# Kernel tuning notes

Measured on AMD Instinct MI355X. Metric: run time of the kernel, lower is better.

The kernel has to match this reference:

```python
import jax, jax.numpy as jnp
import numpy as np

N, E, G = 50000, 800000, 100
H, C = 4, 64


def _gatv2(x, src, dst, ea, Wl, bl, Wr, br, We, att, bias):
    # PyG GATv2Conv: x_l = lin_l(x) (source side), x_r = lin_r(x) (target side)
    xl = (x @ Wl + bl).reshape(-1, H, C)
    xr = (x @ Wr + br).reshape(-1, H, C)
    e = (ea @ We).reshape(-1, H, C)               # [E,H,C]
    m = jax.nn.leaky_relu(xl[src] + xr[dst] + e, negative_slope=0.2)
    alpha = jnp.einsum('ehc,hc->eh', m, att)      # [E,H]
    amax = jax.ops.segment_max(alpha, dst, num_segments=N)
    amax = jnp.where(jnp.isfinite(amax), amax, jnp.float32(0.0))
    ex = jnp.exp(alpha - amax[dst])
    denom = jax.ops.segment_sum(ex, dst, num_segments=N)
    a = ex / (denom[dst] + jnp.float32(1e-16))    # segment softmax over in-edges
    out = jax.ops.segment_sum(xl[src] * a[..., None], dst, num_segments=N)
    return out.reshape(N, H * C) + bias


def setup_inputs() -> dict:
    key = jax.random.key(0)
    ks = jax.random.split(key, 24)
    lin = lambda k, i, o: (jax.random.normal(k, (i, o), jnp.float32) / np.sqrt(i).astype(np.float32))
    x = jax.random.normal(ks[0], (N, 8), jnp.float32)
    edge_index = jnp.stack([jax.random.randint(ks[1], (E,), 0, N),
                            jax.random.randint(ks[2], (E,), 0, N)])
    edge_attr = jax.random.normal(ks[3], (E, 1), jnp.float32)
    batch = jnp.sort(jax.random.randint(ks[4], (N,), 0, G))
    return dict(
        x=x, edge_index=edge_index, edge_attr=edge_attr, batch=batch,
        enc_W=lin(ks[5], 8, 64), enc_b=jnp.zeros((64,), jnp.float32),
        g1_Wl=lin(ks[6], 64, 256), g1_bl=jnp.zeros((256,), jnp.float32),
        g1_Wr=lin(ks[7], 64, 256), g1_br=jnp.zeros((256,), jnp.float32),
        g1_We=lin(ks[8], 1, 256),
        g1_att=jax.random.normal(ks[9], (H, C), jnp.float32) / np.sqrt(C).astype(np.float32),
        g1_bias=jnp.zeros((256,), jnp.float32),
        g2_Wl=lin(ks[10], 256, 256), g2_bl=jnp.zeros((256,), jnp.float32),
        g2_Wr=lin(ks[11], 256, 256), g2_br=jnp.zeros((256,), jnp.float32),
        g2_We=lin(ks[12], 1, 256),
        g2_att=jax.random.normal(ks[13], (H, C), jnp.float32) / np.sqrt(C).astype(np.float32),
        g2_bias=jnp.zeros((256,), jnp.float32),
        p1_W=lin(ks[14], 256, 128), p1_b=jnp.zeros((128,), jnp.float32),
        ln_g=jnp.ones((128,), jnp.float32), ln_b=jnp.zeros((128,), jnp.float32),
        p2_W=lin(ks[15], 128, 64), p2_b=jnp.zeros((64,), jnp.float32),
    )


def reference(x, edge_index, edge_attr, batch,
              enc_W, enc_b,
              g1_Wl, g1_bl, g1_Wr, g1_br, g1_We, g1_att, g1_bias,
              g2_Wl, g2_bl, g2_Wr, g2_br, g2_We, g2_att, g2_bias,
              p1_W, p1_b, ln_g, ln_b, p2_W, p2_b):
    src, dst = edge_index[0], edge_index[1]
    h = jax.nn.relu(x @ enc_W + enc_b)
    h = jax.nn.relu(_gatv2(h, src, dst, edge_attr, g1_Wl, g1_bl, g1_Wr, g1_br, g1_We, g1_att, g1_bias))
    h = jax.nn.relu(_gatv2(h, src, dst, edge_attr, g2_Wl, g2_bl, g2_Wr, g2_br, g2_We, g2_att, g2_bias))
    # global mean pool over graphs
    sums = jax.ops.segment_sum(h, batch, num_segments=G)
    cnt = jax.ops.segment_sum(jnp.ones((N, 1), h.dtype), batch, num_segments=G)
    p = sums / jnp.maximum(cnt, jnp.float32(1.0))
    # post MLP (dropout is identity in eval)
    z = p @ p1_W + p1_b
    mu = jnp.mean(z, axis=-1, keepdims=True)
    var = jnp.mean(jnp.square(z - mu), axis=-1, keepdims=True)
    z = (z - mu) * jax.lax.rsqrt(var + jnp.float32(1e-5)) * ln_g + ln_b
    z = jax.nn.relu(z)
    return jax.nn.relu(z @ p2_W + p2_b)
```

## Files before the change

kernel.cpp:

```cpp
#include <hip/hip_runtime.h>
#include <hip/hip_fp16.h>

#define NH 4
#define CH 64

__global__ void encoder_kernel(const float* __restrict__ x, const float* __restrict__ W,
                               const float* __restrict__ b, float* __restrict__ h, int N) {
  int idx = blockIdx.x * blockDim.x + threadIdx.x;
  if (idx >= N * 64) return;
  int n = idx >> 6, j = idx & 63;
  const float* xp = x + n * 8;
  float acc = b[j];
#pragma unroll
  for (int k = 0; k < 8; ++k) acc = fmaf(xp[k], W[k * 64 + j], acc);
  h[idx] = fmaxf(acc, 0.0f);
}

template <int K>
__global__ void lin_lr_kernel(const float* __restrict__ h,
                              const float* __restrict__ Wl, const float* __restrict__ bl,
                              const float* __restrict__ Wr, const float* __restrict__ br,
                              __half* __restrict__ xl, float* __restrict__ xr, int N) {
  __shared__ float hs[8][K];
  int n0 = blockIdx.x * 8;
  int j = threadIdx.x;
  int nmax = N - n0; if (nmax > 8) nmax = 8;
  for (int idx = j; idx < nmax * K; idx += 256) {
    int m = idx / K, k = idx % K;
    hs[m][k] = h[(size_t)(n0 + m) * K + k];
  }
  __syncthreads();
  float accl[8], accr[8];
  float bjl = bl[j], bjr = br[j];
#pragma unroll
  for (int m = 0; m < 8; ++m) { accl[m] = bjl; accr[m] = bjr; }
  for (int k = 0; k < K; ++k) {
    float wl = Wl[k * 256 + j];
    float wr = Wr[k * 256 + j];
#pragma unroll
    for (int m = 0; m < 8; ++m) {
      accl[m] = fmaf(hs[m][k], wl, accl[m]);
      accr[m] = fmaf(hs[m][k], wr, accr[m]);
    }
  }
  for (int m = 0; m < nmax; ++m) {
    xl[(size_t)(n0 + m) * 256 + j] = __float2half_rn(accl[m]);
    xr[(size_t)(n0 + m) * 256 + j] = accr[m];
  }
}

__global__ void hist_kernel(const int* __restrict__ dst, int* __restrict__ deg, int E) {
  int e = blockIdx.x * blockDim.x + threadIdx.x;
  if (e < E) atomicAdd(&deg[dst[e]], 1);
}

__global__ void scan_partial_kernel(const int* __restrict__ deg, int* __restrict__ partial, int N) {
  __shared__ int sm[256];
  int t = threadIdx.x;
  int i = blockIdx.x * 256 + t;
  sm[t] = (i < N) ? deg[i] : 0;
  __syncthreads();
#pragma unroll
  for (int s = 128; s > 0; s >>= 1) {
    if (t < s) sm[t] += sm[t + s];
    __syncthreads();
  }
  if (t == 0) partial[blockIdx.x] = sm[0];
}

__global__ void scan_offsets_kernel(int* __restrict__ partial, int nb) {
  __shared__ int sm[256];
  int t = threadIdx.x;
  int v = (t < nb) ? partial[t] : 0;
  sm[t] = v;
  __syncthreads();
#pragma unroll
  for (int off = 1; off < 256; off <<= 1) {
    int a = (t >= off) ? sm[t - off] : 0;
    __syncthreads();
    sm[t] += a;
    __syncthreads();
  }
  if (t < nb) partial[t] = sm[t] - v;
}

__global__ void scan_final_kernel(const int* __restrict__ deg, const int* __restrict__ partial,
                                  int* __restrict__ rowptr, int* __restrict__ cursor, int N, int E) {
  __shared__ int sm[256];
  int t = threadIdx.x;
  int i = blockIdx.x * 256 + t;
  int v = (i < N) ? deg[i] : 0;
  sm[t] = v;
  __syncthreads();
#pragma unroll
  for (int off = 1; off < 256; off <<= 1) {
    int a = (t >= off) ? sm[t - off] : 0;
    __syncthreads();
    sm[t] += a;
    __syncthreads();
  }
  if (i < N) {
    int ex = partial[blockIdx.x] + sm[t] - v;
    rowptr[i] = ex;
    cursor[i] = ex;
  }
  if (i == 0) rowptr[N] = E;
}

__global__ void scatter_build_kernel(const int* __restrict__ src, const int* __restrict__ dst,
                                     const float* __restrict__ ea, int* __restrict__ cursor,
                                     int* __restrict__ srcs, float* __restrict__ eas, int E) {
  int e = blockIdx.x * blockDim.x + threadIdx.x;
  if (e >= E) return;
  int d = dst[e];
  int pos = atomicAdd(&cursor[d], 1);
  srcs[pos] = src[e];
  eas[pos] = ea[e];
}

__device__ __forceinline__ float4 ldxl(const uint2* __restrict__ xlh, int s, int lane) {
  uint2 r = xlh[(size_t)s * 64 + lane];
  __half2 a = *reinterpret_cast<const __half2*>(&r.x);
  __half2 b = *reinterpret_cast<const __half2*>(&r.y);
  float2 fa = __half22float2(a);
  float2 fb = __half22float2(b);
  return make_float4(fa.x, fa.y, fb.x, fb.y);
}

__device__ __forceinline__ void edge_accum(const float4 xlv, const float eav,
                                           const float4 xr4, const float4 We4, const float4 at4,
                                           float4& acc, float& denom) {
  float4 v;
  v.x = fmaf(eav, We4.x, xlv.x + xr4.x);
  v.y = fmaf(eav, We4.y, xlv.y + xr4.y);
  v.z = fmaf(eav, We4.z, xlv.z + xr4.z);
  v.w = fmaf(eav, We4.w, xlv.w + xr4.w);
  v.x = (v.x >= 0.f) ? v.x : 0.2f * v.x;
  v.y = (v.y >= 0.f) ? v.y : 0.2f * v.y;
  v.z = (v.z >= 0.f) ? v.z : 0.2f * v.z;
  v.w = (v.w >= 0.f) ? v.w : 0.2f * v.w;
  float p = v.x * at4.x + v.y * at4.y + v.z * at4.z + v.w * at4.w;
  p += __shfl_xor(p, 1, 64);
  p += __shfl_xor(p, 2, 64);
  p += __shfl_xor(p, 4, 64);
  p += __shfl_xor(p, 8, 64);
  float ex = __expf(p);
  denom += ex;
  acc.x = fmaf(ex, xlv.x, acc.x);
  acc.y = fmaf(ex, xlv.y, acc.y);
  acc.z = fmaf(ex, xlv.z, acc.z);
  acc.w = fmaf(ex, xlv.w, acc.w);
}

template <bool POOL>
__global__ void gat_aggregate_kernel(const int* __restrict__ rowptr,
                                     const int* __restrict__ srcs,
                                     const float* __restrict__ eas,
                                     const __half* __restrict__ xl,
                                     const float* __restrict__ xr,
                                     const float* __restrict__ We,
                                     const float* __restrict__ att,
                                     const float* __restrict__ bias,
                                     float* __restrict__ out,
                                     const int* __restrict__ batch,
                                     float* __restrict__ sums,
                                     float* __restrict__ cnt,
                                     int N) {
  int d = (int)((blockIdx.x * (size_t)blockDim.x + threadIdx.x) >> 6);
  int lane = threadIdx.x & 63;
  if (d >= N) return;
  const uint2* xlh = (const uint2*)xl;
  float4 xr4 = ((const float4*)xr)[(size_t)d * 64 + lane];
  float4 We4 = ((const float4*)We)[lane];
  float4 at4 = ((const float4*)att)[lane];
  int beg = rowptr[d], end = rowptr[d + 1];
  float4 acc = {0.f, 0.f, 0.f, 0.f};
  float denom = 0.f;
  int i = beg;
  for (; i + 7 < end; i += 8) {
    int s[8]; float ev[8];
#pragma unroll
    for (int k = 0; k < 8; ++k) { s[k] = srcs[i + k]; ev[k] = eas[i + k]; }
    float4 a[8];
#pragma unroll
    for (int k = 0; k < 8; ++k) a[k] = ldxl(xlh, s[k], lane);
#pragma unroll
    for (int k = 0; k < 8; ++k) edge_accum(a[k], ev[k], xr4, We4, at4, acc, denom);
  }
  for (; i + 3 < end; i += 4) {
    int s[4]; float ev[4];
#pragma unroll
    for (int k = 0; k < 4; ++k) { s[k] = srcs[i + k]; ev[k] = eas[i + k]; }
    float4 a[4];
#pragma unroll
    for (int k = 0; k < 4; ++k) a[k] = ldxl(xlh, s[k], lane);
#pragma unroll
    for (int k = 0; k < 4; ++k) edge_accum(a[k], ev[k], xr4, We4, at4, acc, denom);
  }
  for (; i < end; ++i) {
    float4 a0 = ldxl(xlh, srcs[i], lane);
    edge_accum(a0, eas[i], xr4, We4, at4, acc, denom);
  }
  float inv = 1.f / (denom + 1e-16f);
  float4 b4 = ((const float4*)bias)[lane];
  float4 o;
  o.x = fmaxf(fmaf(acc.x, inv, b4.x), 0.f);
  o.y = fmaxf(fmaf(acc.y, inv, b4.y), 0.f);
  o.z = fmaxf(fmaf(acc.z, inv, b4.z), 0.f);
  o.w = fmaxf(fmaf(acc.w, inv, b4.w), 0.f);
  if (POOL) {
    int g = batch[d];
    float* sg = sums + (size_t)g * 256 + lane * 4;
    atomicAdd(sg + 0, o.x);
    atomicAdd(sg + 1, o.y);
    atomicAdd(sg + 2, o.z);
    atomicAdd(sg + 3, o.w);
    if (lane == 0) atomicAdd(&cnt[g], 1.0f);
  } else {
    ((float4*)out)[(size_t)d * 64 + lane] = o;
  }
}

__global__ void mlp_kernel(const float* __restrict__ sums, const float* __restrict__ cnt,
                           const float* __restrict__ p1W, const float* __restrict__ p1b,
                           const float* __restrict__ lng, const float* __restrict__ lnb,
                           const float* __restrict__ p2W, const float* __restrict__ p2b,
                           float* __restrict__ outp, int G) {
  __shared__ float p[256];
  __shared__ float z[128];
  __shared__ float wsum[2];
  __shared__ float wsum2[2];
  int g = blockIdx.x;
  int t = threadIdx.x;
  float c = fmaxf(cnt[g], 1.0f);
  p[t] = sums[(size_t)g * 256 + t] / c;
  p[t + 128] = sums[(size_t)g * 256 + t + 128] / c;
  __syncthreads();
  float acc = p1b[t];
  for (int k = 0; k < 256; ++k) acc = fmaf(p[k], p1W[k * 128 + t], acc);
  float v = acc;
#pragma unroll
  for (int off = 32; off > 0; off >>= 1) v += __shfl_xor(v, off, 64);
  if ((t & 63) == 0) wsum[t >> 6] = v;
  __syncthreads();
  float mu = (wsum[0] + wsum[1]) * (1.0f / 128.0f);
  float dv = acc - mu;
  float vv = dv * dv;
#pragma unroll
  for (int off = 32; off > 0; off >>= 1) vv += __shfl_xor(vv, off, 64);
  if ((t & 63) == 0) wsum2[t >> 6] = vv;
  __syncthreads();
  float var = (wsum2[0] + wsum2[1]) * (1.0f / 128.0f);
  float zv = dv * rsqrtf(var + 1e-5f) * lng[t] + lnb[t];
  z[t] = fmaxf(zv, 0.0f);
  __syncthreads();
  if (t < 64) {
    float o = p2b[t];
    for (int k = 0; k < 128; ++k) o = fmaf(z[k], p2W[k * 64 + t], o);
    outp[(size_t)g * 64 + t] = fmaxf(o, 0.0f);
  }
}

extern "C" void kernel_launch(void* const* d_in, const int* in_sizes, int n_in,
                              void* d_out, int out_size, void* d_ws, size_t ws_size,
                              hipStream_t stream) {
  const float* x      = (const float*)d_in[0];
  const int*   ei     = (const int*)d_in[1];
  const float* ea     = (const float*)d_in[2];
  const int*   batch  = (const int*)d_in[3];
  const float* enc_W  = (const float*)d_in[4];
  const float* enc_b  = (const float*)d_in[5];
  const float* Wl1    = (const float*)d_in[6];
  const float* bl1    = (const float*)d_in[7];
  const float* Wr1    = (const float*)d_in[8];
  const float* br1    = (const float*)d_in[9];
  const float* We1    = (const float*)d_in[10];
  const float* att1   = (const float*)d_in[11];
  const float* bias1  = (const float*)d_in[12];
  const float* Wl2    = (const float*)d_in[13];
  const float* bl2    = (const float*)d_in[14];
  const float* Wr2    = (const float*)d_in[15];
  const float* br2    = (const float*)d_in[16];
  const float* We2    = (const float*)d_in[17];
  const float* att2   = (const float*)d_in[18];
  const float* bias2  = (const float*)d_in[19];
  const float* p1W    = (const float*)d_in[20];
  const float* p1b    = (const float*)d_in[21];
  const float* lng    = (const float*)d_in[22];
  const float* lnb    = (const float*)d_in[23];
  const float* p2W    = (const float*)d_in[24];
  const float* p2b    = (const float*)d_in[25];
  float* outp = (float*)d_out;

  int N = in_sizes[0] / 8;
  int E = in_sizes[2];
  int G = out_size / 64;
  const int* src = ei;
  const int* dst = ei + E;
  int nb = (N + 255) / 256;

  float* ws      = (float*)d_ws;
  float* h0      = ws;
  float* B0      = h0     + (size_t)N * 64;
  float* B1      = B0     + (size_t)N * 256;
  float* B2      = B1     + (size_t)N * 256;
  float* eas     = B2     + (size_t)N * 256;
  float* sums    = eas    + (size_t)E;
  float* cnt     = sums   + (size_t)G * 256;
  int*   srcs    = (int*)(cnt + G);
  int*   rowptr  = srcs + (size_t)E;
  int*   cursor  = rowptr + (size_t)(N + 1);
  int*   partial = cursor + (size_t)N;
  __half* B0h    = (__half*)B0;

  encoder_kernel<<<(N * 64 + 255) / 256, 256, 0, stream>>>(x, enc_W, enc_b, h0, N);

  hipMemsetAsync(cursor, 0, (size_t)N * sizeof(int), stream);
  hist_kernel<<<(E + 255) / 256, 256, 0, stream>>>(dst, cursor, E);
  scan_partial_kernel<<<nb, 256, 0, stream>>>(cursor, partial, N);
  scan_offsets_kernel<<<1, 256, 0, stream>>>(partial, nb);
  scan_final_kernel<<<nb, 256, 0, stream>>>(cursor, partial, rowptr, cursor, N, E);
  scatter_build_kernel<<<(E + 255) / 256, 256, 0, stream>>>(src, dst, ea, cursor, srcs, eas, E);

  lin_lr_kernel<64><<<(N + 7) / 8, 256, 0, stream>>>(h0, Wl1, bl1, Wr1, br1, B0h, B1, N);
  gat_aggregate_kernel<false><<<(N + 3) / 4, 256, 0, stream>>>(
      rowptr, srcs, eas, B0h, B1, We1, att1, bias1, B2, nullptr, nullptr, nullptr, N);

  lin_lr_kernel<256><<<(N + 7) / 8, 256, 0, stream>>>(B2, Wl2, bl2, Wr2, br2, B0h, B1, N);
  hipMemsetAsync(sums, 0, ((size_t)G * 256 + G) * sizeof(float), stream);
  gat_aggregate_kernel<true><<<(N + 3) / 4, 256, 0, stream>>>(
      rowptr, srcs, eas, B0h, B1, We2, att2, bias2, nullptr, batch, sums, cnt, N);

  mlp_kernel<<<G, 128, 0, stream>>>(sums, cnt, p1W, p1b, lng, lnb, p2W, p2b, outp, G);
}
```

Before: 1.077 ms.

## Partition in-edges by source range and aggregate per partition with reduction

Builds the CSR keyed by (dst, source-partition) so each destination's in-edges are split into eight source-range buckets. A partial kernel processes one bucket per wavefront, so blocks launched together gather from a narrower slice of xl and get better cache locality. It writes normalized fp16 partials and denominators, and a reduce kernel combines them. xr is also stored in fp16 to cut its traffic. The cost is an extra pass over partial buffers, eight times as many rowptr and histogram entries, a less numerically exact softmax without max subtraction, and chunking that depends on workspace size.

New measurement: 1.419 ms. 1.32x slower.

```diff
diff --git a/kernel.cpp b/kernel.cpp
--- a/kernel.cpp
+++ b/kernel.cpp
@@ -3,6 +3,7 @@
 
 #define NH 4
 #define CH 64
+#define PPART 8
 
 __global__ void encoder_kernel(const float* __restrict__ x, const float* __restrict__ W,
                                const float* __restrict__ b, float* __restrict__ h, int N) {
@@ -20,7 +21,7 @@
 __global__ void lin_lr_kernel(const float* __restrict__ h,
                               const float* __restrict__ Wl, const float* __restrict__ bl,
                               const float* __restrict__ Wr, const float* __restrict__ br,
-                              __half* __restrict__ xl, float* __restrict__ xr, int N) {
+                              __half* __restrict__ xl, __half* __restrict__ xr, int N) {
   __shared__ float hs[8][K];
   int n0 = blockIdx.x * 8;
   int j = threadIdx.x;
@@ -45,24 +46,28 @@
   }
   for (int m = 0; m < nmax; ++m) {
     xl[(size_t)(n0 + m) * 256 + j] = __float2half_rn(accl[m]);
-    xr[(size_t)(n0 + m) * 256 + j] = accr[m];
-  }
-}
-
-__global__ void hist_kernel(const int* __restrict__ dst, int* __restrict__ deg, int E) {
+    xr[(size_t)(n0 + m) * 256 + j] = __float2half_rn(accr[m]);
+  }
+}
+
+__global__ void hist2_kernel(const int* __restrict__ src, const int* __restrict__ dst,
+                             int* __restrict__ deg2, int E, int psz) {
   int e = blockIdx.x * blockDim.x + threadIdx.x;
-  if (e < E) atomicAdd(&deg[dst[e]], 1);
-}
-
-__global__ void scan_partial_kernel(const int* __restrict__ deg, int* __restrict__ partial, int N) {
+  if (e < E) atomicAdd(&deg2[dst[e] * PPART + src[e] / psz], 1);
+}
+
+__global__ void scan_partial2_kernel(const int* __restrict__ deg, int* __restrict__ partial, int M) {
   __shared__ int sm[256];
   int t = threadIdx.x;
-  int i = blockIdx.x * 256 + t;
-  sm[t] = (i < N) ? deg[i] : 0;
-  __syncthreads();
-#pragma unroll
-  for (int s = 128; s > 0; s >>= 1) {
-    if (t < s) sm[t] += sm[t + s];
+  int base = blockIdx.x * 2048 + t * 8;
+  int s = 0;
+#pragma unroll
+  for (int k = 0; k < 8; ++k) { int i = base + k; s += (i < M) ? deg[i] : 0; }
+  sm[t] = s;
+  __syncthreads();
+#pragma unroll
+  for (int st = 128; st > 0; st >>= 1) {
+    if (t < st) sm[t] += sm[t + st];
     __syncthreads();
   }
   if (t == 0) partial[blockIdx.x] = sm[0];
@@ -84,13 +89,15 @@
   if (t < nb) partial[t] = sm[t] - v;
 }
 
-__global__ void scan_final_kernel(const int* __restrict__ deg, const int* __restrict__ partial,
-                                  int* __restrict__ rowptr, int* __restrict__ cursor, int N, int E) {
+__global__ void scan_final2_kernel(const int* __restrict__ deg, const int* __restrict__ partial,
+                                   int* __restrict__ rowptr, int* __restrict__ cursor, int M, int E) {
   __shared__ int sm[256];
   int t = threadIdx.x;
-  int i = blockIdx.x * 256 + t;
-  int v = (i < N) ? deg[i] : 0;
-  sm[t] = v;
+  int base = blockIdx.x * 2048 + t * 8;
+  int v[8]; int s = 0;
+#pragma unroll
+  for (int k = 0; k < 8; ++k) { int i = base + k; v[k] = (i < M) ? deg[i] : 0; s += v[k]; }
+  sm[t] = s;
   __syncthreads();
 #pragma unroll
   for (int off = 1; off < 256; off <<= 1) {
@@ -99,32 +106,43 @@
     sm[t] += a;
     __syncthreads();
   }
-  if (i < N) {
-    int ex = partial[blockIdx.x] + sm[t] - v;
-    rowptr[i] = ex;
-    cursor[i] = ex;
-  }
-  if (i == 0) rowptr[N] = E;
-}
-
-__global__ void scatter_build_kernel(const int* __restrict__ src, const int* __restrict__ dst,
-                                     const float* __restrict__ ea, int* __restrict__ cursor,
-                                     int* __restrict__ srcs, float* __restrict__ eas, int E) {
+  int run = partial[blockIdx.x] + sm[t] - s;
+#pragma unroll
+  for (int k = 0; k < 8; ++k) {
+    int i = base + k;
+    if (i < M) { rowptr[i] = run; cursor[i] = run; run += v[k]; }
+  }
+  if (blockIdx.x == 0 && t == 0) rowptr[M] = E;
+}
+
+__global__ void scatter_build2_kernel(const int* __restrict__ src, const int* __restrict__ dst,
+                                      const float* __restrict__ ea, int* __restrict__ cursor,
+                                      int* __restrict__ srcs, float* __restrict__ eas, int E, int psz) {
   int e = blockIdx.x * blockDim.x + threadIdx.x;
   if (e >= E) return;
-  int d = dst[e];
-  int pos = atomicAdd(&cursor[d], 1);
-  srcs[pos] = src[e];
+  int s = src[e];
+  int key = dst[e] * PPART + s / psz;
+  int pos = atomicAdd(&cursor[key], 1);
+  srcs[pos] = s;
   eas[pos] = ea[e];
 }
 
-__device__ __forceinline__ float4 ldxl(const uint2* __restrict__ xlh, int s, int lane) {
-  uint2 r = xlh[(size_t)s * 64 + lane];
+__device__ __forceinline__ float4 ldh4(const uint2* __restrict__ p, size_t idx) {
+  uint2 r = p[idx];
   __half2 a = *reinterpret_cast<const __half2*>(&r.x);
   __half2 b = *reinterpret_cast<const __half2*>(&r.y);
   float2 fa = __half22float2(a);
   float2 fb = __half22float2(b);
   return make_float4(fa.x, fa.y, fb.x, fb.y);
+}
+
+__device__ __forceinline__ uint2 sth4(float4 v) {
+  __half2 a = __floats2half2_rn(v.x, v.y);
+  __half2 b = __floats2half2_rn(v.z, v.w);
+  uint2 r;
+  r.x = *reinterpret_cast<unsigned*>(&a);
+  r.y = *reinterpret_cast<unsigned*>(&b);
+  return r;
 }
 
 __device__ __forceinline__ void edge_accum(const float4 xlv, const float eav,
@@ -152,56 +170,81 @@
   acc.w = fmaf(ex, xlv.w, acc.w);
 }
 
-template <bool POOL>
-__global__ void gat_aggregate_kernel(const int* __restrict__ rowptr,
-                                     const int* __restrict__ srcs,
-                                     const float* __restrict__ eas,
-                                     const __half* __restrict__ xl,
-                                     const float* __restrict__ xr,
-                                     const float* __restrict__ We,
-                                     const float* __restrict__ att,
-                                     const float* __restrict__ bias,
-                                     float* __restrict__ out,
-                                     const int* __restrict__ batch,
-                                     float* __restrict__ sums,
-                                     float* __restrict__ cnt,
-                                     int N) {
-  int d = (int)((blockIdx.x * (size_t)blockDim.x + threadIdx.x) >> 6);
+__global__ void gat_partial_kernel(const int* __restrict__ rowptr2,
+                                   const int* __restrict__ srcs,
+                                   const float* __restrict__ eas,
+                                   const __half* __restrict__ xl,
+                                   const __half* __restrict__ xr,
+                                   const float* __restrict__ We,
+                                   const float* __restrict__ att,
+                                   uint2* __restrict__ Pacc,
+                                   float* __restrict__ denomP,
+                                   int chunk0, int Nc, int cap) {
+  int b = blockIdx.x;
+  int s = b & 7;
+  int nb = b >> 3;
+  int w = threadIdx.x >> 6;
   int lane = threadIdx.x & 63;
-  if (d >= N) return;
+  int ln = nb * 4 + w;
+  if (ln >= Nc) return;
+  int d = chunk0 + ln;
   const uint2* xlh = (const uint2*)xl;
-  float4 xr4 = ((const float4*)xr)[(size_t)d * 64 + lane];
+  const uint2* xrh = (const uint2*)xr;
+  float4 xr4 = ldh4(xrh, (size_t)d * 64 + lane);
   float4 We4 = ((const float4*)We)[lane];
   float4 at4 = ((const float4*)att)[lane];
-  int beg = rowptr[d], end = rowptr[d + 1];
+  int beg = rowptr2[d * PPART + s], end = rowptr2[d * PPART + s + 1];
   float4 acc = {0.f, 0.f, 0.f, 0.f};
   float denom = 0.f;
   int i = beg;
-  for (; i + 7 < end; i += 8) {
-    int s[8]; float ev[8];
-#pragma unroll
-    for (int k = 0; k < 8; ++k) { s[k] = srcs[i + k]; ev[k] = eas[i + k]; }
-    float4 a[8];
-#pragma unroll
-    for (int k = 0; k < 8; ++k) a[k] = ldxl(xlh, s[k], lane);
-#pragma unroll
-    for (int k = 0; k < 8; ++k) edge_accum(a[k], ev[k], xr4, We4, at4, acc, denom);
-  }
-  for (; i + 3 < end; i += 4) {
-    int s[4]; float ev[4];
-#pragma unroll
-    for (int k = 0; k < 4; ++k) { s[k] = srcs[i + k]; ev[k] = eas[i + k]; }
-    float4 a[4];
-#pragma unroll
-    for (int k = 0; k < 4; ++k) a[k] = ldxl(xlh, s[k], lane);
-#pragma unroll
-    for (int k = 0; k < 4; ++k) edge_accum(a[k], ev[k], xr4, We4, at4, acc, denom);
-  }
-  for (; i < end; ++i) {
-    float4 a0 = ldxl(xlh, srcs[i], lane);
+  for (; i + 1 < end; i += 2) {
+    int s0 = srcs[i], s1 = srcs[i + 1];
+    float e0 = eas[i], e1 = eas[i + 1];
+    float4 a0 = ldh4(xlh, (size_t)s0 * 64 + lane);
+    float4 a1 = ldh4(xlh, (size_t)s1 * 64 + lane);
+    edge_accum(a0, e0, xr4, We4, at4, acc, denom);
+    edge_accum(a1, e1, xr4, We4, at4, acc, denom);
+  }
+  if (i < end) {
+    float4 a0 = ldh4(xlh, (size_t)srcs[i] * 64 + lane);
     edge_accum(a0, eas[i], xr4, We4, at4, acc, denom);
   }
-  float inv = 1.f / (denom + 1e-16f);
+  float inv = (denom > 0.f) ? (1.f / denom) : 0.f;
+  float4 m = make_float4(acc.x * inv, acc.y * inv, acc.z * inv, acc.w * inv);
+  size_t slot = (size_t)s * cap + ln;
+  Pacc[slot * 64 + lane] = sth4(m);
+  if ((lane & 15) == 0) denomP[slot * 4 + (lane >> 4)] = denom;
+}
+
+template <bool POOL>
+__global__ void gat_reduce_kernel(const uint2* __restrict__ Pacc,
+                                  const float* __restrict__ denomP,
+                                  const float* __restrict__ bias,
+                                  float* __restrict__ out,
+                                  const int* __restrict__ batch,
+                                  float* __restrict__ sums,
+                                  float* __restrict__ cnt,
+                                  int chunk0, int Nc, int cap) {
+  int w = threadIdx.x >> 6;
+  int lane = threadIdx.x & 63;
+  int ln = blockIdx.x * 4 + w;
+  if (ln >= Nc) return;
+  int d = chunk0 + ln;
+  int h = lane >> 4;
+  float4 acc = {0.f, 0.f, 0.f, 0.f};
+  float D = 0.f;
+#pragma unroll
+  for (int s = 0; s < PPART; ++s) {
+    size_t slot = (size_t)s * cap + ln;
+    float ds = denomP[slot * 4 + h];
+    float4 m = ldh4(Pacc, slot * 64 + lane);
+    D += ds;
+    acc.x = fmaf(ds, m.x, acc.x);
+    acc.y = fmaf(ds, m.y, acc.y);
+    acc.z = fmaf(ds, m.z, acc.z);
+    acc.w = fmaf(ds, m.w, acc.w);
+  }
+  float inv = 1.f / (D + 1e-16f);
   float4 b4 = ((const float4*)bias)[lane];
   float4 o;
   o.x = fmaxf(fmaf(acc.x, inv, b4.x), 0.f);
@@ -297,39 +340,61 @@
   int G = out_size / 64;
   const int* src = ei;
   const int* dst = ei + E;
-  int nb = (N + 255) / 256;
+  int M = N * PPART;
+  int psz = (N + PPART - 1) / PPART;
+  int nb2 = (M + 2047) / 2048;
 
   float* ws      = (float*)d_ws;
   float* h0      = ws;
-  float* B0      = h0     + (size_t)N * 64;
-  float* B1      = B0     + (size_t)N * 256;
-  float* B2      = B1     + (size_t)N * 256;
+  __half* xlh    = (__half*)(h0 + (size_t)N * 64);
+  __half* xrh    = (__half*)((float*)xlh + (size_t)N * 128);
+  float* B2      = (float*)xrh + (size_t)N * 128;
   float* eas     = B2     + (size_t)N * 256;
   float* sums    = eas    + (size_t)E;
   float* cnt     = sums   + (size_t)G * 256;
   int*   srcs    = (int*)(cnt + G);
-  int*   rowptr  = srcs + (size_t)E;
-  int*   cursor  = rowptr + (size_t)(N + 1);
-  int*   partial = cursor + (size_t)N;
-  __half* B0h    = (__half*)B0;
+  int*   rowptr2 = srcs + (size_t)E;
+  int*   cursor2 = rowptr2 + (size_t)(M + 1);
+  int*   partial = cursor2 + (size_t)M;
+  char*  pbase_c = (char*)(partial + 256);
+  size_t used    = (size_t)(pbase_c - (char*)d_ws);
+  used           = (used + 15) & ~(size_t)15;
+  size_t avail   = (ws_size > used) ? (ws_size - used) : 0;
+  int cap = (int)(avail / 4224);
+  if (cap > N) cap = N;
+  if (cap < 1) cap = 1;
+  uint2* Pacc    = (uint2*)((char*)d_ws + used);
+  float* denomP  = (float*)((char*)Pacc + (size_t)cap * 4096);
 
   encoder_kernel<<<(N * 64 + 255) / 256, 256, 0, stream>>>(x, enc_W, enc_b, h0, N);
 
-  hipMemsetAsync(cursor, 0, (size_t)N * sizeof(int), stream);
-  hist_kernel<<<(E + 255) / 256, 256, 0, stream>>>(dst, cursor, E);
-  scan_partial_kernel<<<nb, 256, 0, stream>>>(cursor, partial, N);
-  scan_offsets_kernel<<<1, 256, 0, stream>>>(partial, nb);
-  scan_final_kernel<<<nb, 256, 0, stream>>>(cursor, partial, rowptr, cursor, N, E);
-  scatter_build_kernel<<<(E + 255) / 256, 256, 0, stream>>>(src, dst, ea, cursor, srcs, eas, E);
-
-  lin_lr_kernel<64><<<(N + 7) / 8, 256, 0, stream>>>(h0, Wl1, bl1, Wr1, br1, B0h, B1, N);
-  gat_aggregate_kernel<false><<<(N + 3) / 4, 256, 0, stream>>>(
-      rowptr, srcs, eas, B0h, B1, We1, att1, bias1, B2, nullptr, nullptr, nullptr, N);
-
-  lin_lr_kernel<256><<<(N + 7) / 8, 256, 0, stream>>>(B2, Wl2, bl2, Wr2, br2, B0h, B1, N);
+  hipMemsetAsync(cursor2, 0, (size_t)M * sizeof(int), stream);
+  hist2_kernel<<<(E + 255) / 256, 256, 0, stream>>>(src, dst, cursor2, E, psz);
+  scan_partial2_kernel<<<nb2, 256, 0, stream>>>(cursor2, partial, M);
+  scan_offsets_kernel<<<1, 256, 0, stream>>>(partial, nb2);
+  scan_final2_kernel<<<nb2, 256, 0, stream>>>(cursor2, partial, rowptr2, cursor2, M, E);
+  scatter_build2_kernel<<<(E + 255) / 256, 256, 0, stream>>>(src, dst, ea, cursor2, srcs, eas, E, psz);
+
+  lin_lr_kernel<64><<<(N + 7) / 8, 256, 0, stream>>>(h0, Wl1, bl1, Wr1, br1, xlh, xrh, N);
+  for (int c0 = 0; c0 < N; c0 += cap) {
+    int Nc = N - c0; if (Nc > cap) Nc = cap;
+    int nblk = (Nc + 3) / 4;
+    gat_partial_kernel<<<nblk * PPART, 256, 0, stream>>>(
+        rowptr2, srcs, eas, xlh, xrh, We1, att1, Pacc, denomP, c0, Nc, cap);
+    gat_reduce_kernel<false><<<nblk, 256, 0, stream>>>(
+        Pacc, denomP, bias1, B2, nullptr, nullptr, nullptr, c0, Nc, cap);
+  }
+
+  lin_lr_kernel<256><<<(N + 7) / 8, 256, 0, stream>>>(B2, Wl2, bl2, Wr2, br2, xlh, xrh, N);
   hipMemsetAsync(sums, 0, ((size_t)G * 256 + G) * sizeof(float), stream);
-  gat_aggregate_kernel<true><<<(N + 3) / 4, 256, 0, stream>>>(
-      rowptr, srcs, eas, B0h, B1, We2, att2, bias2, nullptr, batch, sums, cnt, N);
+  for (int c0 = 0; c0 < N; c0 += cap) {
+    int Nc = N - c0; if (Nc > cap) Nc = cap;
+    int nblk = (Nc + 3) / 4;
+    gat_partial_kernel<<<nblk * PPART, 256, 0, stream>>>(
+        rowptr2, srcs, eas, xlh, xrh, We2, att2, Pacc, denomP, c0, Nc, cap);
+    gat_reduce_kernel<true><<<nblk, 256, 0, stream>>>(
+        Pacc, denomP, bias2, nullptr, batch, sums, cnt, c0, Nc, cap);
+  }
 
   mlp_kernel<<<G, 128, 0, stream>>>(sums, cnt, p1W, p1b, lng, lnb, p2W, p2b, outp, G);
 }
```

## Split wavefront into two half-waves processing two edges each with 16-byte fp16 loads

Applied to the files above, without the earlier changes.

The aggregation kernel now assigns each half of the 64-lane wavefront to a different in-edge, and each lane handles 8 channels through a single 16-byte load of fp16 xl. This halves the number of serial edge iterations per destination, and the two partial accumulators are combined with a cross-half shuffle at the end. xr is also stored in fp16, which halves its write and read traffic at some cost in precision. Odd-degree tails are handled with a mask on the upper half.

After: 1.072 ms. No clear change (-0.5%).

```diff
diff --git a/kernel.cpp b/kernel.cpp
--- a/kernel.cpp
+++ b/kernel.cpp
@@ -20,7 +20,7 @@
 __global__ void lin_lr_kernel(const float* __restrict__ h,
                               const float* __restrict__ Wl, const float* __restrict__ bl,
                               const float* __restrict__ Wr, const float* __restrict__ br,
-                              __half* __restrict__ xl, float* __restrict__ xr, int N) {
+                              __half* __restrict__ xl, __half* __restrict__ xr, int N) {
   __shared__ float hs[8][K];
   int n0 = blockIdx.x * 8;
   int j = threadIdx.x;
@@ -45,7 +45,7 @@
   }
   for (int m = 0; m < nmax; ++m) {
     xl[(size_t)(n0 + m) * 256 + j] = __float2half_rn(accl[m]);
-    xr[(size_t)(n0 + m) * 256 + j] = accr[m];
+    xr[(size_t)(n0 + m) * 256 + j] = __float2half_rn(accr[m]);
   }
 }
 
@@ -118,106 +118,124 @@
   eas[pos] = ea[e];
 }
 
-__device__ __forceinline__ float4 ldxl(const uint2* __restrict__ xlh, int s, int lane) {
-  uint2 r = xlh[(size_t)s * 64 + lane];
-  __half2 a = *reinterpret_cast<const __half2*>(&r.x);
-  __half2 b = *reinterpret_cast<const __half2*>(&r.y);
-  float2 fa = __half22float2(a);
-  float2 fb = __half22float2(b);
-  return make_float4(fa.x, fa.y, fb.x, fb.y);
-}
-
-__device__ __forceinline__ void edge_accum(const float4 xlv, const float eav,
-                                           const float4 xr4, const float4 We4, const float4 at4,
-                                           float4& acc, float& denom) {
-  float4 v;
-  v.x = fmaf(eav, We4.x, xlv.x + xr4.x);
-  v.y = fmaf(eav, We4.y, xlv.y + xr4.y);
-  v.z = fmaf(eav, We4.z, xlv.z + xr4.z);
-  v.w = fmaf(eav, We4.w, xlv.w + xr4.w);
-  v.x = (v.x >= 0.f) ? v.x : 0.2f * v.x;
-  v.y = (v.y >= 0.f) ? v.y : 0.2f * v.y;
-  v.z = (v.z >= 0.f) ? v.z : 0.2f * v.z;
-  v.w = (v.w >= 0.f) ? v.w : 0.2f * v.w;
-  float p = v.x * at4.x + v.y * at4.y + v.z * at4.z + v.w * at4.w;
+__device__ __forceinline__ void unpack8(const uint4 r, float o[8]) {
+  const __half2* hp = reinterpret_cast<const __half2*>(&r);
+#pragma unroll
+  for (int k = 0; k < 4; ++k) {
+    float2 f = __half22float2(hp[k]);
+    o[2 * k] = f.x; o[2 * k + 1] = f.y;
+  }
+}
+
+__device__ __forceinline__ void pair_accum(const uint4 raw, const float eav, const float mask,
+                                           const float xr8[8], const float We8[8], const float at8[8],
+                                           float acc[8], float& den) {
+  float xlv[8];
+  unpack8(raw, xlv);
+  float p = 0.f;
+#pragma unroll
+  for (int c = 0; c < 8; ++c) {
+    float v = fmaf(eav, We8[c], xlv[c] + xr8[c]);
+    v = (v >= 0.f) ? v : 0.2f * v;
+    p = fmaf(v, at8[c], p);
+  }
   p += __shfl_xor(p, 1, 64);
   p += __shfl_xor(p, 2, 64);
   p += __shfl_xor(p, 4, 64);
-  p += __shfl_xor(p, 8, 64);
-  float ex = __expf(p);
-  denom += ex;
-  acc.x = fmaf(ex, xlv.x, acc.x);
-  acc.y = fmaf(ex, xlv.y, acc.y);
-  acc.z = fmaf(ex, xlv.z, acc.z);
-  acc.w = fmaf(ex, xlv.w, acc.w);
+  float ex = __expf(p) * mask;
+  den += ex;
+#pragma unroll
+  for (int c = 0; c < 8; ++c) acc[c] = fmaf(ex, xlv[c], acc[c]);
 }
 
 template <bool POOL>
-__global__ void gat_aggregate_kernel(const int* __restrict__ rowptr,
-                                     const int* __restrict__ srcs,
-                                     const float* __restrict__ eas,
-                                     const __half* __restrict__ xl,
-                                     const float* __restrict__ xr,
-                                     const float* __restrict__ We,
-                                     const float* __restrict__ att,
-                                     const float* __restrict__ bias,
-                                     float* __restrict__ out,
-                                     const int* __restrict__ batch,
-                                     float* __restrict__ sums,
-                                     float* __restrict__ cnt,
-                                     int N) {
+__global__ __launch_bounds__(256)
+void gat_aggregate_kernel(const int* __restrict__ rowptr,
+                          const int* __restrict__ srcs,
+                          const float* __restrict__ eas,
+                          const __half* __restrict__ xl,
+                          const __half* __restrict__ xr,
+                          const float* __restrict__ We,
+                          const float* __restrict__ att,
+                          const float* __restrict__ bias,
+                          float* __restrict__ out,
+                          const int* __restrict__ batch,
+                          float* __restrict__ sums,
+                          float* __restrict__ cnt,
+                          int N) {
   int d = (int)((blockIdx.x * (size_t)blockDim.x + threadIdx.x) >> 6);
   int lane = threadIdx.x & 63;
   if (d >= N) return;
-  const uint2* xlh = (const uint2*)xl;
-  float4 xr4 = ((const float4*)xr)[(size_t)d * 64 + lane];
-  float4 We4 = ((const float4*)We)[lane];
-  float4 at4 = ((const float4*)att)[lane];
+  int lq = lane & 31;
+  bool lo = (lane < 32);
+  const uint4* xlh8 = (const uint4*)xl;
+  const uint4* xrh8 = (const uint4*)xr;
+  float xr8[8];
+  { uint4 r = xrh8[(size_t)d * 32 + lq]; unpack8(r, xr8); }
+  float We8[8], at8[8];
+#pragma unroll
+  for (int k = 0; k < 8; ++k) { We8[k] = We[lq * 8 + k]; at8[k] = att[lq * 8 + k]; }
   int beg = rowptr[d], end = rowptr[d + 1];
-  float4 acc = {0.f, 0.f, 0.f, 0.f};
-  float denom = 0.f;
+  float acc[8];
+#pragma unroll
+  for (int c = 0; c < 8; ++c) acc[c] = 0.f;
+  float den = 0.f;
+  int pend = beg + ((end - beg) & ~1);
   int i = beg;
-  for (; i + 7 < end; i += 8) {
-    int s[8]; float ev[8];
-#pragma unroll
-    for (int k = 0; k < 8; ++k) { s[k] = srcs[i + k]; ev[k] = eas[i + k]; }
-    float4 a[8];
-#pragma unroll
-    for (int k = 0; k < 8; ++k) a[k] = ldxl(xlh, s[k], lane);
-#pragma unroll
-    for (int k = 0; k < 8; ++k) edge_accum(a[k], ev[k], xr4, We4, at4, acc, denom);
-  }
-  for (; i + 3 < end; i += 4) {
-    int s[4]; float ev[4];
-#pragma unroll
-    for (int k = 0; k < 4; ++k) { s[k] = srcs[i + k]; ev[k] = eas[i + k]; }
-    float4 a[4];
-#pragma unroll
-    for (int k = 0; k < 4; ++k) a[k] = ldxl(xlh, s[k], lane);
-#pragma unroll
-    for (int k = 0; k < 4; ++k) edge_accum(a[k], ev[k], xr4, We4, at4, acc, denom);
-  }
-  for (; i < end; ++i) {
-    float4 a0 = ldxl(xlh, srcs[i], lane);
-    edge_accum(a0, eas[i], xr4, We4, at4, acc, denom);
-  }
-  float inv = 1.f / (denom + 1e-16f);
-  float4 b4 = ((const float4*)bias)[lane];
+  for (; i + 7 < pend; i += 8) {
+    int s0 = srcs[i],     s1 = srcs[i + 1], s2 = srcs[i + 2], s3 = srcs[i + 3];
+    int s4 = srcs[i + 4], s5 = srcs[i + 5], s6 = srcs[i + 6], s7 = srcs[i + 7];
+    int a0 = lo ? s0 : s1, a1 = lo ? s2 : s3, a2 = lo ? s4 : s5, a3 = lo ? s6 : s7;
+    uint4 r0 = xlh8[(size_t)a0 * 32 + lq];
+    uint4 r1 = xlh8[(size_t)a1 * 32 + lq];
+    uint4 r2 = xlh8[(size_t)a2 * 32 + lq];
+    uint4 r3 = xlh8[(size_t)a3 * 32 + lq];
+    float e0 = eas[i],     e1 = eas[i + 1], e2 = eas[i + 2], e3 = eas[i + 3];
+    float e4 = eas[i + 4], e5 = eas[i + 5], e6 = eas[i + 6], e7 = eas[i + 7];
+    float f0 = lo ? e0 : e1, f1 = lo ? e2 : e3, f2 = lo ? e4 : e5, f3 = lo ? e6 : e7;
+    pair_accum(r0, f0, 1.f, xr8, We8, at8, acc, den);
+    pair_accum(r1, f1, 1.f, xr8, We8, at8, acc, den);
+    pair_accum(r2, f2, 1.f, xr8, We8, at8, acc, den);
+    pair_accum(r3, f3, 1.f, xr8, We8, at8, acc, den);
+  }
+  for (; i < pend; i += 2) {
+    int s0 = srcs[i], s1 = srcs[i + 1];
+    int a0 = lo ? s0 : s1;
+    uint4 r0 = xlh8[(size_t)a0 * 32 + lq];
+    float f0 = lo ? eas[i] : eas[i + 1];
+    pair_accum(r0, f0, 1.f, xr8, We8, at8, acc, den);
+  }
+  if (pend < end) {
+    int s0 = srcs[end - 1];
+    uint4 r0 = xlh8[(size_t)s0 * 32 + lq];
+    float f0 = eas[end - 1];
+    pair_accum(r0, f0, lo ? 1.f : 0.f, xr8, We8, at8, acc, den);
+  }
+  den += __shfl_xor(den, 32, 64);
+#pragma unroll
+  for (int c = 0; c < 8; ++c) acc[c] += __shfl_xor(acc[c], 32, 64);
+  float inv = 1.f / (den + 1e-16f);
+  int half = lane >> 5;
+  float c0 = half ? acc[4] : acc[0];
+  float c1 = half ? acc[5] : acc[1];
+  float c2 = half ? acc[6] : acc[2];
+  float c3 = half ? acc[7] : acc[3];
+  float4 b4 = ((const float4*)bias)[lq * 2 + half];
   float4 o;
-  o.x = fmaxf(fmaf(acc.x, inv, b4.x), 0.f);
-  o.y = fmaxf(fmaf(acc.y, inv, b4.y), 0.f);
-  o.z = fmaxf(fmaf(acc.z, inv, b4.z), 0.f);
-  o.w = fmaxf(fmaf(acc.w, inv, b4.w), 0.f);
+  o.x = fmaxf(fmaf(c0, inv, b4.x), 0.f);
+  o.y = fmaxf(fmaf(c1, inv, b4.y), 0.f);
+  o.z = fmaxf(fmaf(c2, inv, b4.z), 0.f);
+  o.w = fmaxf(fmaf(c3, inv, b4.w), 0.f);
   if (POOL) {
     int g = batch[d];
-    float* sg = sums + (size_t)g * 256 + lane * 4;
+    float* sg = sums + (size_t)g * 256 + lq * 8 + half * 4;
     atomicAdd(sg + 0, o.x);
     atomicAdd(sg + 1, o.y);
     atomicAdd(sg + 2, o.z);
     atomicAdd(sg + 3, o.w);
     if (lane == 0) atomicAdd(&cnt[g], 1.0f);
   } else {
-    ((float4*)out)[(size_t)d * 64 + lane] = o;
+    ((float4*)out)[(size_t)d * 64 + lq * 2 + half] = o;
   }
 }
 
@@ -301,9 +319,9 @@
 
   float* ws      = (float*)d_ws;
   float* h0      = ws;
-  float* B0      = h0     + (size_t)N * 64;
-  float* B1      = B0     + (size_t)N * 256;
-  float* B2      = B1     + (size_t)N * 256;
+  __half* xlh    = (__half*)(h0 + (size_t)N * 64);
+  __half* xrh    = (__half*)((float*)xlh + (size_t)N * 128);
+  float* B2      = (float*)xrh + (size_t)N * 128;
   float* eas     = B2     + (size_t)N * 256;
   float* sums    = eas    + (size_t)E;
   float* cnt     = sums   + (size_t)G * 256;
@@ -311,7 +329,6 @@
   int*   rowptr  = srcs + (size_t)E;
   int*   cursor  = rowptr + (size_t)(N + 1);
   int*   partial = cursor + (size_t)N;
-  __half* B0h    = (__half*)B0;
 
   encoder_kernel<<<(N * 64 + 255) / 256, 256, 0, stream>>>(x, enc_W, enc_b, h0, N);
 
@@ -322,14 +339,14 @@
   scan_final_kernel<<<nb, 256, 0, stream>>>(cursor, partial, rowptr, cursor, N, E);
   scatter_build_kernel<<<(E + 255) / 256, 256, 0, stream>>>(src, dst, ea, cursor, srcs, eas, E);
 
-  lin_lr_kernel<64><<<(N + 7) / 8, 256, 0, stream>>>(h0, Wl1, bl1, Wr1, br1, B0h, B1, N);
+  lin_lr_kernel<64><<<(N + 7) / 8, 256, 0, stream>>>(h0, Wl1, bl1, Wr1, br1, xlh, xrh, N);
   gat_aggregate_kernel<false><<<(N + 3) / 4, 256, 0, stream>>>(
-      rowptr, srcs, eas, B0h, B1, We1, att1, bias1, B2, nullptr, nullptr, nullptr, N);
-
-  lin_lr_kernel<256><<<(N + 7) / 8, 256, 0, stream>>>(B2, Wl2, bl2, Wr2, br2, B0h, B1, N);
+      rowptr, srcs, eas, xlh, xrh, We1, att1, bias1, B2, nullptr, nullptr, nullptr, N);
+
+  lin_lr_kernel<256><<<(N + 7) / 8, 256, 0, stream>>>(B2, Wl2, bl2, Wr2, br2, xlh, xrh, N);
   hipMemsetAsync(sums, 0, ((size_t)G * 256 + G) * sizeof(float), stream);
   gat_aggregate_kernel<true><<<(N + 3) / 4, 256, 0, stream>>>(
-      rowptr, srcs, eas, B0h, B1, We2, att2, bias2, nullptr, batch, sums, cnt, N);
+      rowptr, srcs, eas, xlh, xrh, We2, att2, bias2, nullptr, batch, sums, cnt, N);
 
   mlp_kernel<<<G, 128, 0, stream>>>(sums, cnt, p1W, p1b, lng, lnb, p2W, p2b, outp, G);
 }
```
